# Performance work log

Hardware: AMD Instinct MI355X
Metric: run time of the kernel (lower is better)

Reference implementation:

```python
import jax, jax.numpy as jnp
import numpy as np

B, N = 8, 128          # batch, nodes
D = 256                # message_size (== resized node/edge feature size)
LH = 512               # link_hidden_size
P = 3                  # propagate_layers
C = 117                # hoi_classes
DE, DN = 200, 100      # raw edge / node feature sizes


def setup_inputs() -> dict:
    key = jax.random.key(0)
    ks = jax.random.split(key, 12)
    g = lambda k, sh, s=0.05: jax.random.normal(k, sh, dtype=jnp.float32) * s
    return {
        "edge_features": jax.random.normal(ks[0], (B, N, N, DE), dtype=jnp.float32),
        "node_features": jax.random.normal(ks[1], (B, N, DN), dtype=jnp.float32),
        # feature resize linears
        "W_er": g(ks[2], (D, DE)), "b_er": jnp.zeros((D,), jnp.float32),
        "W_nr": g(ks[3], (D, DN)), "b_nr": jnp.zeros((D,), jnp.float32),
        # link function: GraphConv = per-edge MLP (1x1 convs), last layer -> 1 channel
        "Wl1": g(ks[4], (LH, D)), "bl1": jnp.zeros((LH,), jnp.float32),
        "Wl2": g(ks[5], (LH, LH)), "bl2": jnp.zeros((LH,), jnp.float32),
        "Wl3": g(ks[6], (1, LH)), "bl3": jnp.zeros((1,), jnp.float32),
        # message function: Linear(concat(h_w, e_vw)) + ReLU
        "W_m": g(ks[7], (D, 2 * D)), "b_m": jnp.zeros((D,), jnp.float32),
        # GRU update (single layer): torch GRU weight layout [r; z; n]
        "W_ih": g(ks[8], (3 * D, D)), "b_ih": jnp.zeros((3 * D,), jnp.float32),
        "W_hh": g(ks[9], (3 * D, D)), "b_hh": jnp.zeros((3 * D,), jnp.float32),
        # readout fc
        "W_r": g(ks[10], (C, D)), "b_r": jnp.zeros((C,), jnp.float32),
    }


def reference(edge_features, node_features, W_er, b_er, W_nr, b_nr,
              Wl1, bl1, Wl2, bl2, Wl3, bl3, W_m, b_m,
              W_ih, b_ih, W_hh, b_hh, W_r, b_r):
    # resize raw features to message size
    ef = edge_features @ W_er.T + b_er           # [B,N_i,N_w,D] (target i, source w)
    h = node_features @ W_nr.T + b_nr            # [B,N,D] node hidden states

    e_state = ef                                  # hidden edge state fed to link fun
    pred_adj = None
    for _ in range(P):
        # link function: per-edge MLP (equivalent to 1x1 Conv2d stack), 1-channel out
        x = jax.nn.relu(e_state @ Wl1.T + bl1)
        x = jax.nn.relu(x @ Wl2.T + bl2)
        pred_adj = (x @ Wl3.T + bl3)[..., 0]      # [B,N,N] pre-sigmoid adjacency
        sig = jax.nn.sigmoid(pred_adj)

        # messages m(i<-w) = relu(Linear([h_w ; e_{i,w}])), gated by sigmoid adj
        hw = jnp.broadcast_to(h[:, None, :, :], ef.shape)  # [B,N_i,N_w,D]
        M = jax.nn.relu(jnp.concatenate([hw, ef], axis=-1) @ W_m.T + b_m)
        M = sig[..., None] * M                    # [B,N_i,N_w,D]

        # torch code writes m_v into hidden_edge_states[...][:, :, :, i] -> transpose (i,w)
        e_state = jnp.transpose(M, (0, 2, 1, 3))

        # aggregate over sources, GRU single-step update (input=m, hidden=h)
        m = M.sum(axis=2)                         # [B,N,D]
        gi = m @ W_ih.T + b_ih
        gh = h @ W_hh.T + b_hh
        r = jax.nn.sigmoid(gi[..., :D] + gh[..., :D])
        z = jax.nn.sigmoid(gi[..., D:2 * D] + gh[..., D:2 * D])
        n = jnp.tanh(gi[..., 2 * D:] + r * gh[..., 2 * D:])
        h = (1.0 - z) * n + z * h

    pred_node_labels = h @ W_r.T + b_r            # [B,N,C]
    return pred_adj, pred_node_labels
```

## Files before the change

kernel.cpp:

```cpp
#include <hip/hip_runtime.h>
#include <math.h>

typedef unsigned short u16;
typedef __attribute__((ext_vector_type(8))) short short8;
typedef __attribute__((ext_vector_type(4))) short short4v;
typedef __attribute__((ext_vector_type(4))) float floatx4;

__device__ __forceinline__ float bf2f(u16 u) {
  union { unsigned int i; float f; } v; v.i = ((unsigned int)u) << 16; return v.f;
}
__device__ __forceinline__ u16 f2bf(float f) {
  union { unsigned int i; float f; } v; v.f = f;
  unsigned int i = v.i;
  unsigned int lsb = (i >> 16) & 1u;
  i += 0x7fffu + lsb;
  return (u16)(i >> 16);
}

__global__ __launch_bounds__(256, 2)
void fused_front_k(const float* __restrict__ edge, const u16* __restrict__ Wcomb,
                   const float* __restrict__ b_er, const float* __restrict__ cmb,
                   u16* __restrict__ es, u16* __restrict__ Em)
{
  __shared__ __align__(16) u16 As[64 * 232];
  const int tid  = threadIdx.x;
  const int lane = tid & 63;
  const int wv   = tid >> 6;
  const int q    = lane >> 4;
  const int cl   = lane & 15;
  const long r0  = (long)blockIdx.x * 64;

  for (int z = tid; z < 64 * 24; z += 256) {
    const int zr = z / 24;
    As[zr * 232 + 200 + (z - zr * 24)] = 0;
  }
  const float4* src = (const float4*)(edge + r0 * 200);
  for (int it = tid; it < 3200; it += 256) {
    const float4 v = src[it];
    const int row = it / 50;
    const int c4  = it - row * 50;
    u16 t[4] = { f2bf(v.x), f2bf(v.y), f2bf(v.z), f2bf(v.w) };
    *(short4v*)&As[row * 232 + c4 * 4] = *(short4v*)t;
  }
  __syncthreads();

  floatx4 acc[4][8];
#pragma unroll
  for (int mi = 0; mi < 4; ++mi)
#pragma unroll
    for (int ni = 0; ni < 8; ++ni)
      acc[mi][ni] = (floatx4){0.f, 0.f, 0.f, 0.f};

  short8 b0[8], b1[8];
#pragma unroll
  for (int ni = 0; ni < 8; ++ni)
    b0[ni] = *(const short8*)(Wcomb + (long)(wv * 128 + ni * 16 + cl) * 224 + q * 8);
#pragma unroll
  for (int ks = 0; ks < 7; ++ks) {
    short8* bc = (ks & 1) ? b1 : b0;
    short8* bn = (ks & 1) ? b0 : b1;
    if (ks < 6) {
      const int kb = (ks + 1) * 32;
#pragma unroll
      for (int ni = 0; ni < 8; ++ni)
        bn[ni] = *(const short8*)(Wcomb + (long)(wv * 128 + ni * 16 + cl) * 224 + kb + q * 8);
    }
    short8 a[4];
#pragma unroll
    for (int mi = 0; mi < 4; ++mi)
      a[mi] = *(const short8*)&As[(mi * 16 + cl) * 232 + ks * 32 + q * 8];
#pragma unroll
    for (int mi = 0; mi < 4; ++mi)
#pragma unroll
      for (int ni = 0; ni < 8; ++ni)
        acc[mi][ni] = __builtin_amdgcn_mfma_f32_16x16x32_bf16(a[mi], bc[ni], acc[mi][ni], 0, 0, 0);
  }

  const bool is_ef   = (wv < 2);
  const float* bias  = is_ef ? b_er : cmb;
  u16* dst           = is_ef ? es : Em;
  const int colbase  = (wv & 1) * 128;
#pragma unroll
  for (int mi = 0; mi < 4; ++mi)
#pragma unroll
    for (int ni = 0; ni < 8; ++ni) {
      const int col = colbase + ni * 16 + cl;
      const float bb = bias[col];
#pragma unroll
      for (int r = 0; r < 4; ++r) {
        const int row = mi * 16 + q * 4 + r;
        dst[(r0 + row) * 256 + col] = f2bf(acc[mi][ni][r] + bb);
      }
    }
}

__global__ __launch_bounds__(512, 2)
void link_k(const u16* __restrict__ es, const u16* __restrict__ Wl1b,
            const float* __restrict__ bl1, const u16* __restrict__ Wl2b,
            const float* __restrict__ bl2, const float* __restrict__ wl3,
            const float* __restrict__ bl3, float* __restrict__ adj)
{
  __shared__ __align__(16) u16 x1b[128 * 512];
  const int tid  = threadIdx.x;
  const int lane = tid & 63;
  const int wv   = tid >> 6;
  const int q    = lane >> 4;
  const int cl   = lane & 15;
  const int nw0  = wv * 64;
  const long r0  = (long)blockIdx.x * 128;

  {
    const short8* gsrc = (const short8*)(es + r0 * 256);
#pragma unroll
    for (int i = 0; i < 8; ++i) {
      const int g   = tid + i * 512;
      const int row = g >> 5;
      const int c   = g & 31;
      const short8 v = gsrc[g];
      *(short8*)&x1b[row * 256 + ((c ^ (row & 15)) << 3)] = v;
    }
  }

  floatx4 acc[8][4];
#pragma unroll
  for (int mi = 0; mi < 8; ++mi)
#pragma unroll
    for (int ni = 0; ni < 4; ++ni)
      acc[mi][ni] = (floatx4){0.f, 0.f, 0.f, 0.f};

  short8 b0[4], b1[4];
#pragma unroll
  for (int ni = 0; ni < 4; ++ni)
    b0[ni] = *(const short8*)(Wl1b + (nw0 + ni * 16 + cl) * 256 + q * 8);
  __syncthreads();

  {
#pragma unroll
    for (int ks = 0; ks < 8; ++ks) {
      short8* bc = (ks & 1) ? b1 : b0;
      short8* bn = (ks & 1) ? b0 : b1;
      if (ks < 7) {
        const int kb = (ks + 1) * 32;
#pragma unroll
        for (int ni = 0; ni < 4; ++ni)
          bn[ni] = *(const short8*)(Wl1b + (nw0 + ni * 16 + cl) * 256 + kb + q * 8);
      }
      short8 a[8];
#pragma unroll
      for (int mi = 0; mi < 8; ++mi) {
        const int row = mi * 16 + cl;
        a[mi] = *(const short8*)&x1b[row * 256 + (((ks * 4 + q) ^ cl) << 3)];
      }
#pragma unroll
      for (int mi = 0; mi < 8; ++mi)
#pragma unroll
        for (int ni = 0; ni < 4; ++ni)
          acc[mi][ni] = __builtin_amdgcn_mfma_f32_16x16x32_bf16(a[mi], bc[ni], acc[mi][ni], 0, 0, 0);
    }
  }
  __syncthreads();

#pragma unroll
  for (int mi = 0; mi < 8; ++mi)
#pragma unroll
    for (int ni = 0; ni < 4; ++ni) {
      const int col = nw0 + ni * 16 + cl;
      const float bb = bl1[col];
      const int chunk = col >> 3;
#pragma unroll
      for (int r = 0; r < 4; ++r) {
        const int row = mi * 16 + q * 4 + r;
        const float v = fmaxf(acc[mi][ni][r] + bb, 0.f);
        x1b[row * 512 + (((chunk ^ (row & 15)) << 3) | (col & 7))] = f2bf(v);
      }
    }
#pragma unroll
  for (int mi = 0; mi < 8; ++mi)
#pragma unroll
    for (int ni = 0; ni < 4; ++ni)
      acc[mi][ni] = (floatx4){0.f, 0.f, 0.f, 0.f};
  __syncthreads();

  {
    short8 c0[4], c1[4];
#pragma unroll
    for (int ni = 0; ni < 4; ++ni)
      c0[ni] = *(const short8*)(Wl2b + (nw0 + ni * 16 + cl) * 512 + q * 8);
#pragma unroll
    for (int ks = 0; ks < 16; ++ks) {
      short8* bc = (ks & 1) ? c1 : c0;
      short8* bn = (ks & 1) ? c0 : c1;
      if (ks < 15) {
        const int kb = (ks + 1) * 32;
#pragma unroll
        for (int ni = 0; ni < 4; ++ni)
          bn[ni] = *(const short8*)(Wl2b + (nw0 + ni * 16 + cl) * 512 + kb + q * 8);
      }
      short8 a[8];
#pragma unroll
      for (int mi = 0; mi < 8; ++mi) {
        const int row = mi * 16 + cl;
        a[mi] = *(const short8*)&x1b[row * 512 + (((ks * 4 + q) ^ cl) << 3)];
      }
#pragma unroll
      for (int mi = 0; mi < 8; ++mi)
#pragma unroll
        for (int ni = 0; ni < 4; ++ni)
          acc[mi][ni] = __builtin_amdgcn_mfma_f32_16x16x32_bf16(a[mi], bc[ni], acc[mi][ni], 0, 0, 0);
    }
  }

  float pv[8][4];
#pragma unroll
  for (int mi = 0; mi < 8; ++mi)
#pragma unroll
    for (int r = 0; r < 4; ++r) pv[mi][r] = 0.f;
#pragma unroll
  for (int mi = 0; mi < 8; ++mi)
#pragma unroll
    for (int ni = 0; ni < 4; ++ni) {
      const int col = nw0 + ni * 16 + cl;
      const float bb = bl2[col];
      const float w3 = wl3[col];
#pragma unroll
      for (int r = 0; r < 4; ++r) {
        const float v = fmaxf(acc[mi][ni][r] + bb, 0.f);
        pv[mi][r] += v * w3;
      }
    }
  __syncthreads();
  float* pf = (float*)x1b;
#pragma unroll
  for (int mi = 0; mi < 8; ++mi)
#pragma unroll
    for (int r = 0; r < 4; ++r) {
      float p = pv[mi][r];
#pragma unroll
      for (int off = 1; off < 16; off <<= 1)
        p += __shfl_xor(p, off, 64);
      if (cl == 0) pf[wv * 128 + mi * 16 + q * 4 + r] = p;
    }
  __syncthreads();
  if (tid < 128) {
    float s = bl3[0];
#pragma unroll
    for (int w = 0; w < 8; ++w) s += pf[w * 128 + tid];
    adj[r0 + tid] = s;
  }
}

__device__ __forceinline__
void gemm_sp_dev(const float* __restrict__ A, const u16* __restrict__ Bh,
                 const u16* __restrict__ Bl, const float* __restrict__ bias,
                 float* __restrict__ C,
                 int N, int K_loop, int K_src, int lda, int ldc,
                 int bx, int by)
{
  __shared__ __align__(16) u16 Ash[128 * 40];
  __shared__ __align__(16) u16 Asl[128 * 40];
  __shared__ __align__(16) u16 Bsh[128 * 40];
  __shared__ __align__(16) u16 Bsl[128 * 40];
  const int tid  = threadIdx.x;
  const int m0   = bx * 128;
  const int n0   = by * 128;
  const int lane = tid & 63;
  const int wv   = tid >> 6;
  const int wm   = wv & 1;
  const int wn   = wv >> 1;
  const int q    = lane >> 4;
  const int cl   = lane & 15;

  floatx4 acc[4][4];
#pragma unroll
  for (int i = 0; i < 4; ++i)
#pragma unroll
    for (int j = 0; j < 4; ++j)
      acc[i][j] = (floatx4){0.f, 0.f, 0.f, 0.f};

  const int srow = tid >> 1;
  const int scol = (tid & 1) * 16;

  for (int kb = 0; kb < K_loop; kb += 32) {
    {
      const long r = (long)(m0 + srow);
      u16* dh = &Ash[srow * 40 + scol];
      u16* dl = &Asl[srow * 40 + scol];
#pragma unroll
      for (int j = 0; j < 16; ++j) {
        int kg = kb + scol + j;
        float v = (kg < K_src) ? A[r * lda + kg] : 0.f;
        u16 hi = f2bf(v);
        dh[j] = hi;
        dl[j] = f2bf(v - bf2f(hi));
      }
    }
    {
      const int n = n0 + srow;
      u16* dh = &Bsh[srow * 40 + scol];
      u16* dl = &Bsl[srow * 40 + scol];
      if (n < N) {
        const short8* sh = (const short8*)(Bh + (long)n * K_loop + kb + scol);
        const short8* sl = (const short8*)(Bl + (long)n * K_loop + kb + scol);
        ((short8*)dh)[0] = sh[0]; ((short8*)dh)[1] = sh[1];
        ((short8*)dl)[0] = sl[0]; ((short8*)dl)[1] = sl[1];
      } else {
#pragma unroll
        for (int j = 0; j < 16; ++j) { dh[j] = 0; dl[j] = 0; }
      }
    }
    __syncthreads();

    short8 ah[4], al[4], bh[4], bl[4];
#pragma unroll
    for (int mi = 0; mi < 4; ++mi) {
      ah[mi] = *(const short8*)&Ash[(wm * 64 + mi * 16 + cl) * 40 + q * 8];
      al[mi] = *(const short8*)&Asl[(wm * 64 + mi * 16 + cl) * 40 + q * 8];
    }
#pragma unroll
    for (int ni = 0; ni < 4; ++ni) {
      bh[ni] = *(const short8*)&Bsh[(wn * 64 + ni * 16 + cl) * 40 + q * 8];
      bl[ni] = *(const short8*)&Bsl[(wn * 64 + ni * 16 + cl) * 40 + q * 8];
    }
#pragma unroll
    for (int mi = 0; mi < 4; ++mi)
#pragma unroll
      for (int ni = 0; ni < 4; ++ni) {
        acc[mi][ni] = __builtin_amdgcn_mfma_f32_16x16x32_bf16(ah[mi], bh[ni], acc[mi][ni], 0, 0, 0);
        acc[mi][ni] = __builtin_amdgcn_mfma_f32_16x16x32_bf16(al[mi], bh[ni], acc[mi][ni], 0, 0, 0);
        acc[mi][ni] = __builtin_amdgcn_mfma_f32_16x16x32_bf16(ah[mi], bl[ni], acc[mi][ni], 0, 0, 0);
      }
    __syncthreads();
  }

#pragma unroll
  for (int mi = 0; mi < 4; ++mi) {
    const int row = m0 + wm * 64 + mi * 16 + q * 4;
#pragma unroll
    for (int ni = 0; ni < 4; ++ni) {
      const int col = n0 + wn * 64 + ni * 16 + cl;
      if (col < N) {
        const float b = bias ? bias[col] : 0.f;
#pragma unroll
        for (int r = 0; r < 4; ++r) {
          float v = acc[mi][ni][r] + b;
          C[(long)(row + r) * ldc + col] = v;
        }
      }
    }
  }
}

__global__ __launch_bounds__(256, 2)
void gemm_sp_k(const float* __restrict__ A, const u16* __restrict__ Bh,
               const u16* __restrict__ Bl, const float* __restrict__ bias,
               float* __restrict__ C,
               int N, int K_loop, int K_src, int lda, int ldc)
{
  gemm_sp_dev(A, Bh, Bl, bias, C, N, K_loop, K_src, lda, ldc,
              blockIdx.x, blockIdx.y);
}

__global__ __launch_bounds__(256, 2)
void gemm_hm_gh_k(const float* __restrict__ hbuf,
                  const u16* __restrict__ Wmh_h, const u16* __restrict__ Wmh_l,
                  const u16* __restrict__ Whh_h, const u16* __restrict__ Whh_l,
                  const float* __restrict__ b_hh,
                  float* __restrict__ Hm, float* __restrict__ gh)
{
  if (blockIdx.z == 0) {
    if (blockIdx.y >= 2) return;
    gemm_sp_dev(hbuf, Wmh_h, Wmh_l, nullptr, Hm, 256, 256, 256, 256, 256,
                blockIdx.x, blockIdx.y);
  } else {
    gemm_sp_dev(hbuf, Whh_h, Whh_l, b_hh, gh, 768, 256, 256, 256, 768,
                blockIdx.x, blockIdx.y);
  }
}

__device__ __forceinline__
void cast_pad_dev(u16* __restrict__ dst, const float* __restrict__ src,
                  int rows, int sc, int dc, int stride, int idx)
{
  if (idx >= rows * dc) return;
  int r = idx / dc, c = idx - r * dc;
  float v = (c < sc) ? src[r * stride + c] : 0.f;
  dst[idx] = f2bf(v);
}

__device__ __forceinline__
void cast_split_dev(u16* __restrict__ dh, u16* __restrict__ dl,
                    const float* __restrict__ src,
                    int rows, int sc, int dc, int stride, int idx)
{
  if (idx >= rows * dc) return;
  int r = idx / dc, c = idx - r * dc;
  float v = (c < sc) ? src[r * stride + c] : 0.f;
  u16 hi = f2bf(v);
  dh[idx] = hi;
  dl[idx] = f2bf(v - bf2f(hi));
}

__global__ __launch_bounds__(256)
void prep_all_k(const float* __restrict__ W_er, const float* __restrict__ Wl1,
                const float* __restrict__ Wl2, const float* __restrict__ W_nr,
                const float* __restrict__ W_m, const float* __restrict__ W_ih,
                const float* __restrict__ W_hh, const float* __restrict__ W_r,
                const float* __restrict__ b_er, const float* __restrict__ b_m,
                u16* __restrict__ Wcomb, u16* __restrict__ Wl1b,
                u16* __restrict__ Wl2b,
                u16* __restrict__ Wnr_h, u16* __restrict__ Wnr_l,
                u16* __restrict__ Wmh_h, u16* __restrict__ Wmh_l,
                u16* __restrict__ Wih_h, u16* __restrict__ Wih_l,
                u16* __restrict__ Whh_h, u16* __restrict__ Whh_l,
                u16* __restrict__ Wr_h, u16* __restrict__ Wr_l,
                float* __restrict__ cmb)
{
  const int j = blockIdx.y;
  if (j == 8) {
    if (blockIdx.x >= 256) return;
    const int o = blockIdx.x;
    const int t = threadIdx.x;
    __shared__ float wme[256];
    wme[t] = W_m[o * 512 + 256 + t];
    __syncthreads();
    if (t < 224) {
      float s = 0.f;
      if (t < 200) {
        for (int c = 0; c < 256; ++c) s += wme[c] * W_er[c * 200 + t];
      }
      Wcomb[(256 + o) * 224 + t] = f2bf(s);
    }
    if (t == 0) {
      float s = 0.f;
      for (int c = 0; c < 256; ++c) s += wme[c] * b_er[c];
      cmb[o] = s + b_m[o];
    }
    return;
  }
  const int idx = blockIdx.x * 256 + threadIdx.x;
  switch (j) {
    case 0: cast_pad_dev(Wcomb, W_er, 256, 200, 224, 200, idx); break;
    case 1: cast_pad_dev(Wl1b, Wl1, 512, 256, 256, 256, idx); break;
    case 2: cast_pad_dev(Wl2b, Wl2, 512, 512, 512, 512, idx); break;
    case 3: cast_split_dev(Wnr_h, Wnr_l, W_nr, 256, 100, 128, 100, idx); break;
    case 4: cast_split_dev(Wmh_h, Wmh_l, W_m, 256, 256, 256, 512, idx); break;
    case 5: cast_split_dev(Wih_h, Wih_l, W_ih, 768, 256, 256, 256, idx); break;
    case 6: cast_split_dev(Whh_h, Whh_l, W_hh, 768, 256, 256, 256, idx); break;
    case 7: cast_split_dev(Wr_h, Wr_l, W_r, 117, 256, 256, 256, idx); break;
  }
}

__global__ __launch_bounds__(256)
void message_k(const u16* __restrict__ Em, const float* __restrict__ Hm,
               const float* __restrict__ adj, u16* __restrict__ es,
               float* __restrict__ msum)
{
  const int b = blockIdx.y, i = blockIdx.x;
  const int tid = threadIdx.x;
  const int c = tid & 31;
  const int g = tid >> 5;
  __shared__ float red[8][256];
  float accv[8] = {0.f, 0.f, 0.f, 0.f, 0.f, 0.f, 0.f, 0.f};
  const long base_bi = ((long)(b * 128 + i)) * 128;
  for (int w0 = 0; w0 < 128; w0 += 8) {
    const int w = w0 + g;
    const float a = adj[base_bi + w];
    const float s = 1.f / (1.f + __expf(-a));
    const short8 ev = *(const short8*)(Em + (base_bi + w) * 256 + c * 8);
    const float* hp = Hm + ((long)(b * 128 + w)) * 256 + c * 8;
    u16 mb[8];
#pragma unroll
    for (int j = 0; j < 8; ++j) {
      float x = bf2f(((const u16*)&ev)[j]) + hp[j];
      x = fmaxf(x, 0.f) * s;
      accv[j] += x;
      mb[j] = f2bf(x);
    }
    *(short8*)(es + (((long)(b * 128 + w)) * 128 + i) * 256 + c * 8) = *(short8*)mb;
  }
#pragma unroll
  for (int j = 0; j < 8; ++j) red[g][c * 8 + j] = accv[j];
  __syncthreads();
  float s = 0.f;
#pragma unroll
  for (int gg = 0; gg < 8; ++gg) s += red[gg][tid];
  msum[((long)(b * 128 + i)) * 256 + tid] = s;
}

__global__ void gru_k(const float* __restrict__ gi, const float* __restrict__ gh,
                      float* __restrict__ h)
{
  const int n = blockIdx.x;
  const int d = threadIdx.x;
  const int base = n * 768;
  const float r  = 1.f / (1.f + __expf(-(gi[base + d] + gh[base + d])));
  const float z  = 1.f / (1.f + __expf(-(gi[base + 256 + d] + gh[base + 256 + d])));
  const float nn = tanhf(gi[base + 512 + d] + r * gh[base + 512 + d]);
  const int hi = n * 256 + d;
  h[hi] = (1.f - z) * nn + z * h[hi];
}

extern "C" void kernel_launch(void* const* d_in, const int* in_sizes, int n_in,
                              void* d_out, int out_size, void* d_ws, size_t ws_size,
                              hipStream_t stream)
{
  const float* edge = (const float*)d_in[0];
  const float* node = (const float*)d_in[1];
  const float* W_er = (const float*)d_in[2];
  const float* b_er = (const float*)d_in[3];
  const float* W_nr = (const float*)d_in[4];
  const float* b_nr = (const float*)d_in[5];
  const float* Wl1  = (const float*)d_in[6];
  const float* bl1  = (const float*)d_in[7];
  const float* Wl2  = (const float*)d_in[8];
  const float* bl2  = (const float*)d_in[9];
  const float* Wl3  = (const float*)d_in[10];
  const float* bl3  = (const float*)d_in[11];
  const float* W_m  = (const float*)d_in[12];
  const float* b_m  = (const float*)d_in[13];
  const float* W_ih = (const float*)d_in[14];
  const float* b_ih = (const float*)d_in[15];
  const float* W_hh = (const float*)d_in[16];
  const float* b_hh = (const float*)d_in[17];
  const float* W_r  = (const float*)d_in[18];
  const float* b_r  = (const float*)d_in[19];
  (void)in_sizes; (void)n_in; (void)out_size; (void)ws_size;

  float* out_adj = (float*)d_out;
  float* out_lab = (float*)d_out + 131072;

  char* ws = (char*)d_ws;
  size_t off = 0;
  auto alloc = [&](size_t bytes) -> void* {
    void* p = ws + off; off += (bytes + 255) & ~(size_t)255; return p;
  };
  const long E = 131072;
  u16*   es   = (u16*)  alloc(E * 256 * 2);
  u16*   Em   = (u16*)  alloc(E * 256 * 2);
  float* Hm   = (float*)alloc(1024 * 256 * 4);
  float* hbuf = (float*)alloc(1024 * 256 * 4);
  float* msum = (float*)alloc(1024 * 256 * 4);
  float* gi   = (float*)alloc(1024 * 768 * 4);
  float* gh   = (float*)alloc(1024 * 768 * 4);
  u16*   Wcomb = (u16*) alloc(512 * 224 * 2);
  u16*   Wl1b = (u16*)  alloc(512 * 256 * 2);
  u16*   Wl2b = (u16*)  alloc(512 * 512 * 2);
  float* cmb  = (float*)alloc(256 * 4);
  u16* Wnr_h = (u16*)alloc(256 * 128 * 2); u16* Wnr_l = (u16*)alloc(256 * 128 * 2);
  u16* Wmh_h = (u16*)alloc(256 * 256 * 2); u16* Wmh_l = (u16*)alloc(256 * 256 * 2);
  u16* Wih_h = (u16*)alloc(768 * 256 * 2); u16* Wih_l = (u16*)alloc(768 * 256 * 2);
  u16* Whh_h = (u16*)alloc(768 * 256 * 2); u16* Whh_l = (u16*)alloc(768 * 256 * 2);
  u16* Wr_h  = (u16*)alloc(117 * 256 * 2); u16* Wr_l  = (u16*)alloc(117 * 256 * 2);

  prep_all_k<<<dim3(1024, 9), 256, 0, stream>>>(
      W_er, Wl1, Wl2, W_nr, W_m, W_ih, W_hh, W_r, b_er, b_m,
      Wcomb, Wl1b, Wl2b, Wnr_h, Wnr_l, Wmh_h, Wmh_l,
      Wih_h, Wih_l, Whh_h, Whh_l, Wr_h, Wr_l, cmb);

  fused_front_k<<<2048, dim3(256), 0, stream>>>(edge, Wcomb, b_er, cmb, es, Em);
  gemm_sp_k<<<dim3(8, 2), dim3(256), 0, stream>>>(
      node, Wnr_h, Wnr_l, b_nr, hbuf, 256, 128, 100, 100, 256);

  for (int p = 0; p < 3; ++p) {
    gemm_hm_gh_k<<<dim3(8, 6, 2), dim3(256), 0, stream>>>(
        hbuf, Wmh_h, Wmh_l, Whh_h, Whh_l, b_hh, Hm, gh);
    link_k<<<1024, dim3(512), 0, stream>>>(es, Wl1b, bl1, Wl2b, bl2, Wl3, bl3, out_adj);
    message_k<<<dim3(128, 8), dim3(256), 0, stream>>>(Em, Hm, out_adj, es, msum);
    gemm_sp_k<<<dim3(8, 6), dim3(256), 0, stream>>>(
        msum, Wih_h, Wih_l, b_ih, gi, 768, 256, 256, 256, 768);
    gru_k<<<1024, 256, 0, stream>>>(gi, gh, hbuf);
  }
  gemm_sp_k<<<dim3(8, 1), dim3(256), 0, stream>>>(
      hbuf, Wr_h, Wr_l, b_r, out_lab, 117, 256, 256, 256, 117);
}
```

Baseline: 924.4 us.

## Fuse message computation into link kernel with double-buffered edge state

```diff
diff --git a/kernel.cpp b/kernel.cpp
--- a/kernel.cpp
+++ b/kernel.cpp
@@ -95,10 +95,13 @@
 }
 
 __global__ __launch_bounds__(512, 2)
-void link_k(const u16* __restrict__ es, const u16* __restrict__ Wl1b,
-            const float* __restrict__ bl1, const u16* __restrict__ Wl2b,
-            const float* __restrict__ bl2, const float* __restrict__ wl3,
-            const float* __restrict__ bl3, float* __restrict__ adj)
+void linkmsg_k(const u16* __restrict__ es, const u16* __restrict__ Wl1b,
+               const float* __restrict__ bl1, const u16* __restrict__ Wl2b,
+               const float* __restrict__ bl2, const float* __restrict__ wl3,
+               const float* __restrict__ bl3, const u16* __restrict__ Em,
+               const float* __restrict__ Hm, float* __restrict__ adj,
+               u16* __restrict__ esn, float* __restrict__ msum,
+               const int write_adj, const int write_es)
 {
   __shared__ __align__(16) u16 x1b[128 * 512];
   const int tid  = threadIdx.x;
@@ -229,7 +232,9 @@
       }
     }
   __syncthreads();
-  float* pf = (float*)x1b;
+  float* pf   = (float*)x1b;
+  float* sigv = pf + 1024;
+  float* red  = pf + 2048;
 #pragma unroll
   for (int mi = 0; mi < 8; ++mi)
 #pragma unroll
@@ -245,7 +250,41 @@
     float s = bl3[0];
 #pragma unroll
     for (int w = 0; w < 8; ++w) s += pf[w * 128 + tid];
-    adj[r0 + tid] = s;
+    if (write_adj) adj[r0 + tid] = s;
+    sigv[tid] = 1.f / (1.f + __expf(-s));
+  }
+  __syncthreads();
+
+  const int b  = (int)(blockIdx.x >> 7);
+  const int i  = (int)(blockIdx.x & 127);
+  const int g  = tid >> 5;
+  const int c8 = (tid & 31) * 8;
+  float msacc[8] = {0.f, 0.f, 0.f, 0.f, 0.f, 0.f, 0.f, 0.f};
+  for (int w0 = 0; w0 < 128; w0 += 16) {
+    const int w = w0 + g;
+    const float s = sigv[w];
+    const short8 ev = *(const short8*)(Em + (r0 + w) * 256 + c8);
+    const float4 h0 = *(const float4*)(Hm + ((long)(b * 128 + w)) * 256 + c8);
+    const float4 h1 = *(const float4*)(Hm + ((long)(b * 128 + w)) * 256 + c8 + 4);
+    const float hv[8] = {h0.x, h0.y, h0.z, h0.w, h1.x, h1.y, h1.z, h1.w};
+    u16 mb[8];
+#pragma unroll
+    for (int j = 0; j < 8; ++j) {
+      float x = fmaxf(bf2f(((const u16*)&ev)[j]) + hv[j], 0.f) * s;
+      msacc[j] += x;
+      mb[j] = f2bf(x);
+    }
+    if (write_es)
+      *(short8*)(esn + (((long)(b * 128 + w)) * 128 + i) * 256 + c8) = *(short8*)mb;
+  }
+#pragma unroll
+  for (int j = 0; j < 8; ++j) red[g * 256 + c8 + j] = msacc[j];
+  __syncthreads();
+  if (tid < 256) {
+    float s = 0.f;
+#pragma unroll
+    for (int gg = 0; gg < 16; ++gg) s += red[gg * 256 + tid];
+    msum[((long)(b * 128 + i)) * 256 + tid] = s;
   }
 }
 
@@ -448,43 +487,6 @@
     case 6: cast_split_dev(Whh_h, Whh_l, W_hh, 768, 256, 256, 256, idx); break;
     case 7: cast_split_dev(Wr_h, Wr_l, W_r, 117, 256, 256, 256, idx); break;
   }
-}
-
-__global__ __launch_bounds__(256)
-void message_k(const u16* __restrict__ Em, const float* __restrict__ Hm,
-               const float* __restrict__ adj, u16* __restrict__ es,
-               float* __restrict__ msum)
-{
-  const int b = blockIdx.y, i = blockIdx.x;
-  const int tid = threadIdx.x;
-  const int c = tid & 31;
-  const int g = tid >> 5;
-  __shared__ float red[8][256];
-  float accv[8] = {0.f, 0.f, 0.f, 0.f, 0.f, 0.f, 0.f, 0.f};
-  const long base_bi = ((long)(b * 128 + i)) * 128;
-  for (int w0 = 0; w0 < 128; w0 += 8) {
-    const int w = w0 + g;
-    const float a = adj[base_bi + w];
-    const float s = 1.f / (1.f + __expf(-a));
-    const short8 ev = *(const short8*)(Em + (base_bi + w) * 256 + c * 8);
-    const float* hp = Hm + ((long)(b * 128 + w)) * 256 + c * 8;
-    u16 mb[8];
-#pragma unroll
-    for (int j = 0; j < 8; ++j) {
-      float x = bf2f(((const u16*)&ev)[j]) + hp[j];
-      x = fmaxf(x, 0.f) * s;
-      accv[j] += x;
-      mb[j] = f2bf(x);
-    }
-    *(short8*)(es + (((long)(b * 128 + w)) * 128 + i) * 256 + c * 8) = *(short8*)mb;
-  }
-#pragma unroll
-  for (int j = 0; j < 8; ++j) red[g][c * 8 + j] = accv[j];
-  __syncthreads();
-  float s = 0.f;
-#pragma unroll
-  for (int gg = 0; gg < 8; ++gg) s += red[gg][tid];
-  msum[((long)(b * 128 + i)) * 256 + tid] = s;
 }
 
 __global__ void gru_k(const float* __restrict__ gi, const float* __restrict__ gh,
@@ -535,7 +537,8 @@
     void* p = ws + off; off += (bytes + 255) & ~(size_t)255; return p;
   };
   const long E = 131072;
-  u16*   es   = (u16*)  alloc(E * 256 * 2);
+  u16*   es0  = (u16*)  alloc(E * 256 * 2);
+  u16*   es1  = (u16*)  alloc(E * 256 * 2);
   u16*   Em   = (u16*)  alloc(E * 256 * 2);
   float* Hm   = (float*)alloc(1024 * 256 * 4);
   float* hbuf = (float*)alloc(1024 * 256 * 4);
@@ -557,15 +560,18 @@
       Wcomb, Wl1b, Wl2b, Wnr_h, Wnr_l, Wmh_h, Wmh_l,
       Wih_h, Wih_l, Whh_h, Whh_l, Wr_h, Wr_l, cmb);
 
-  fused_front_k<<<2048, dim3(256), 0, stream>>>(edge, Wcomb, b_er, cmb, es, Em);
+  fused_front_k<<<2048, dim3(256), 0, stream>>>(edge, Wcomb, b_er, cmb, es0, Em);
   gemm_sp_k<<<dim3(8, 2), dim3(256), 0, stream>>>(
       node, Wnr_h, Wnr_l, b_nr, hbuf, 256, 128, 100, 100, 256);
 
+  u16* esbuf[2] = { es0, es1 };
   for (int p = 0; p < 3; ++p) {
     gemm_hm_gh_k<<<dim3(8, 6, 2), dim3(256), 0, stream>>>(
         hbuf, Wmh_h, Wmh_l, Whh_h, Whh_l, b_hh, Hm, gh);
-    link_k<<<1024, dim3(512), 0, stream>>>(es, Wl1b, bl1, Wl2b, bl2, Wl3, bl3, out_adj);
-    message_k<<<dim3(128, 8), dim3(256), 0, stream>>>(Em, Hm, out_adj, es, msum);
+    linkmsg_k<<<1024, dim3(512), 0, stream>>>(
+        esbuf[p & 1], Wl1b, bl1, Wl2b, bl2, Wl3, bl3,
+        Em, Hm, out_adj, esbuf[(p + 1) & 1], msum,
+        (p == 2) ? 1 : 0, (p < 2) ? 1 : 0);
     gemm_sp_k<<<dim3(8, 6), dim3(256), 0, stream>>>(
         msum, Wih_h, Wih_l, b_ih, gi, 768, 256, 256, 256, 768);
     gru_k<<<1024, 256, 0, stream>>>(gi, gh, hbuf);
```

Result: no change. 918.4 us (-0.6%).
